# Kernel optimization log

Hardware: AMD Instinct MI355X
Metric: run time of the kernel (lower is better)

## Reference

```python
import jax, jax.numpy as jnp
import numpy as np

B, N, H, W = 8, 16384, 64, 64
CTX, OUT, ST = 32, 2, 1
HID = [516, 256, 128, 64, 32, 16]
IN_SIZE = CTX + 2 + ST + OUT  # 37


def _bilinear_sample(img, coord):
    """torch F.grid_sample, mode=bilinear, padding=zeros, align_corners=False.
    img: [B,C,H,W]; coord: [B,N,2] (x,y in [-1,1]). Returns [B,C,N]."""
    _, _, Hh, Ww = img.shape
    gx = (coord[..., 0] + 1.0) * (Ww * 0.5) - 0.5
    gy = (coord[..., 1] + 1.0) * (Hh * 0.5) - 0.5
    x0 = jnp.floor(gx)
    y0 = jnp.floor(gy)
    wx1 = gx - x0
    wy1 = gy - y0

    def tap(xi, yi, w):
        valid = (xi >= 0) & (xi < Ww) & (yi >= 0) & (yi < Hh)
        xc = jnp.clip(xi, 0, Ww - 1).astype(jnp.int32)
        yc = jnp.clip(yi, 0, Hh - 1).astype(jnp.int32)
        vals = jax.vmap(lambda im, y, x: im[:, y, x])(img, yc, xc)  # [B,C,N]
        return vals * (w * valid)[:, None, :]

    return (tap(x0, y0, (1 - wx1) * (1 - wy1))
            + tap(x0 + 1, y0, wx1 * (1 - wy1))
            + tap(x0, y0 + 1, (1 - wx1) * wy1)
            + tap(x0 + 1, y0 + 1, wx1 * wy1))


def _layer_shapes():
    shapes = [(IN_SIZE, HID[0])]
    for i in range(len(HID) - 1):
        shapes.append((HID[i] + IN_SIZE, HID[i + 1]))
    shapes.append((HID[-1], OUT))
    return shapes


def setup_inputs():
    key = jax.random.key(0)
    ks = jax.random.split(key, 4 + 7)
    inp = {
        "lr_fields": jax.random.normal(ks[0], (B, OUT, H, W), jnp.float32),
        "context_grid": jax.random.normal(ks[1], (B, CTX, H, W), jnp.float32),
        "hr_eps": jax.random.normal(ks[2], (B, H, W), jnp.float32),
        "coord": jax.random.uniform(ks[3], (B, N, 2), jnp.float32, -1.0, 1.0),
    }
    for j, (fi, fo) in enumerate(_layer_shapes()):
        inp[f"W{j}"] = jax.random.normal(ks[4 + j], (fi, fo), jnp.float32) / np.sqrt(fi)
        inp[f"b{j}"] = jnp.zeros((fo,), jnp.float32)
    return inp


def reference(lr_fields, context_grid, hr_eps, coord,
              W0, b0, W1, b1, W2, b2, W3, b3, W4, b4, W5, b5, W6, b6):
    # original permutes (0,1,3,2) before grid_sample -> swap spatial axes
    ctx_pts = _bilinear_sample(jnp.swapaxes(context_grid, 2, 3), coord)  # [B,CTX,N]
    lr_pts = _bilinear_sample(jnp.swapaxes(lr_fields, 2, 3), coord)      # [B,OUT,N]
    eps_pts = _bilinear_sample(jnp.swapaxes(hr_eps[:, None], 2, 3), coord)  # [B,1,N]
    x_in = jnp.concatenate([
        jnp.transpose(ctx_pts, (0, 2, 1)),
        coord,
        jnp.transpose(lr_pts, (0, 2, 1)),
        jnp.transpose(eps_pts, (0, 2, 1)),
    ], axis=2)  # [B,N,37]
    x = jax.nn.relu(x_in @ W0 + b0)
    for Wl, bl in ((W1, b1), (W2, b2), (W3, b3), (W4, b4), (W5, b5)):
        x = jax.nn.relu(jnp.concatenate([x, x_in], axis=2) @ Wl + bl)
    return x @ W6 + b6  # [B,N,2]
```

## Files before the change

### kernel.cpp

```cpp
#include <hip/hip_runtime.h>


#define NTH     1024
#define NWAVES  16
#define MPTS    64
#define MTILES  (MPTS / 16)
#define SROW    616
#define XIN_OFF 0
#define HSEG    64
#define NPOINTS (8 * 16384)
#define GRIDX   (NPOINTS / MPTS)
#define LDSBYTES (MPTS * SROW * 2)
#define CLSTRIDE 38
#define CLOFF   524288

typedef short          short8  __attribute__((ext_vector_type(8)));
typedef short          short4v __attribute__((ext_vector_type(4)));
typedef float          f32x4   __attribute__((ext_vector_type(4)));
typedef unsigned short u16;

__device__ __forceinline__ u16 f2bf(float f) {
    unsigned int u = __builtin_bit_cast(unsigned int, f);
    u += 0x7fffu + ((u >> 16) & 1u);
    return (u16)(u >> 16);
}

__constant__ int pk_base8[8] = {0, 4224, 23680, 28800, 30336, 30848, 31040, 31104};
__constant__ int pk_ks[7]    = {2, 19, 10, 6, 4, 3, 1};
__constant__ int pk_khp[7]   = {0, 544, 256, 128, 64, 32, 32};
__constant__ int pk_kact[7]  = {0, 516, 256, 128, 64, 32, 16};
__constant__ int pk_nact[7]  = {516, 256, 128, 64, 32, 16, 2};

struct WPtrs { const float* W[7]; };

__global__ void pack_weights(WPtrs wp, u16* __restrict__ out)
{
    const int f = blockIdx.x * blockDim.x + threadIdx.x;
    if (f >= 31104) return;
    int l = 0;
    while (l < 6 && f >= pk_base8[l + 1]) ++l;
    const int r    = f - pk_base8[l];
    const int lane = r & 63;
    const int t    = r >> 6;
    const int ks   = pk_ks[l];
    const int s    = t % ks;
    const int nt   = t / ks;
    const int n    = nt * 16 + (lane & 15);
    const int k0   = s * 32 + (lane >> 4) * 8;
    const int nact = pk_nact[l];
    const int khp  = pk_khp[l];
    const int kact = pk_kact[l];
    const float* W = wp.W[l];

    union { short8 v; u16 e[8]; } frag;
#pragma unroll
    for (int j = 0; j < 8; ++j) {
        const int k = k0 + j;
        float v = 0.0f;
        if (n < nact) {
            if (k < khp) {
                if (k < kact) v = W[k * nact + n];
            } else {
                const int xr = k - khp;
                if (xr < 37) v = W[(kact + xr) * nact + n];
            }
        }
        frag.e[j] = f2bf(v);
    }
    *(short8*)(out + (size_t)f * 8) = frag.v;
}

struct RPk { const float* ctx; const float* lr; const float* eps; float* cl; };

__global__ void repack_cl(RPk q)
{
    __shared__ float ls[64 * CLSTRIDE];
    const int b = blockIdx.x >> 6;
    const int x = blockIdx.x & 63;
    for (int i = threadIdx.x; i < 64 * CLSTRIDE; i += 256) ls[i] = 0.f;
    __syncthreads();
    for (int i = threadIdx.x; i < 35 * 64; i += 256) {
        const int c = i / 64, y = i % 64;
        float v; int slot;
        if (c < 32)      { v = q.ctx[(((size_t)b * 32 + c) * 64 + x) * 64 + y]; slot = c; }
        else if (c < 34) { v = q.lr [(((size_t)b * 2 + (c - 32)) * 64 + x) * 64 + y]; slot = 34 + (c - 32); }
        else             { v = q.eps[(((size_t)b) * 64 + x) * 64 + y];          slot = 36; }
        ls[y * CLSTRIDE + slot] = v;
    }
    __syncthreads();
    float* out = q.cl + ((size_t)b * 64 + x) * 64 * CLSTRIDE;
    for (int i = threadIdx.x; i < 64 * CLSTRIDE; i += 256) out[i] = ls[i];
}

struct MainParams {
    const float* lr;
    const float* ctx;
    const float* eps;
    const float* coord;
    const float* Bb[7];
    const u16*   wpack;
    const float* cl;
    int          clok;
    float*       out;
};

template<int NACT, bool RELU>
__device__ __forceinline__ void store_nt(const f32x4* accm,
                                         const float* __restrict__ bias,
                                         u16* __restrict__ s_act,
                                         int nt, int mbase, int lm, int lq)
{
    const int bn = nt * 16 + lq * 4;
    float bv[4];
    if (bn + 4 <= NACT) {
        const f32x4 b4 = *(const f32x4*)(bias + bn);
        bv[0] = b4[0]; bv[1] = b4[1]; bv[2] = b4[2]; bv[3] = b4[3];
    } else {
#pragma unroll
        for (int r = 0; r < 4; ++r)
            bv[r] = (bn + r < NACT) ? bias[bn + r] : 0.f;
    }
#pragma unroll
    for (int m = 0; m < 2; ++m) {
        short4v o;
#pragma unroll
        for (int r = 0; r < 4; ++r) {
            float v = accm[m][r] + bv[r];
            if (RELU) v = fmaxf(v, 0.f);
            o[r] = (short)f2bf(v);
        }
        *(short4v*)(s_act + (size_t)((mbase + m) * 16 + lm) * SROW + HSEG + bn) = o;
    }
}

template<int KHP, int NT, int NACT, int LBASE,
         bool XIN, bool RELU, bool GOUT, bool IPBAR>
__device__ __forceinline__ void mlayer(const u16* __restrict__ wpack,
                                       const float* __restrict__ bias,
                                       u16* __restrict__ s_act,
                                       float* __restrict__ gout, int p0,
                                       int wave, int lane)
{
    constexpr int KHS = KHP / 32;
    constexpr int KS  = KHS + (XIN ? 2 : 0);
    const int lm = lane & 15;
    const int lq = lane >> 4;
    const int mg = wave & 1;
    const int ng = wave >> 1;
    const int mbase = mg * 2;

    const u16* arow0 = s_act + (size_t)((mbase * 16) + lm) * SROW + lq * 8;
    const u16* arow1 = arow0 + (size_t)16 * SROW;
    const u16* wl = wpack + LBASE + lane * 8;

#define ABOFF(s_) (((s_) < KHS) ? (HSEG + (s_) * 32) : (XIN_OFF + ((s_) - KHS) * 32))

    if constexpr (IPBAR) {
        const int nt0 = ng, nt1 = ng + 8;
        const bool act0 = nt0 < NT;
        const bool act1 = nt1 < NT;
        f32x4 acc[2][2];
#pragma unroll
        for (int i = 0; i < 2; ++i)
#pragma unroll
            for (int m = 0; m < 2; ++m)
                acc[i][m] = (f32x4){0.f, 0.f, 0.f, 0.f};

        if (act0) {
            const u16* bp0 = wl + (size_t)nt0 * KS * 512;
            const u16* bp1 = wl + (size_t)nt1 * KS * 512;
#pragma unroll
            for (int s = 0; s < KS; ++s) {
                const int ab = ABOFF(s);
                const short8 a0 = *(const short8*)(arow0 + ab);
                const short8 a1 = *(const short8*)(arow1 + ab);
                const short8 w0 = *(const short8*)(bp0 + (size_t)s * 512);
                acc[0][0] = __builtin_amdgcn_mfma_f32_16x16x32_bf16(w0, a0, acc[0][0], 0, 0, 0);
                acc[0][1] = __builtin_amdgcn_mfma_f32_16x16x32_bf16(w0, a1, acc[0][1], 0, 0, 0);
                if (act1) {
                    const short8 w1 = *(const short8*)(bp1 + (size_t)s * 512);
                    acc[1][0] = __builtin_amdgcn_mfma_f32_16x16x32_bf16(w1, a0, acc[1][0], 0, 0, 0);
                    acc[1][1] = __builtin_amdgcn_mfma_f32_16x16x32_bf16(w1, a1, acc[1][1], 0, 0, 0);
                }
            }
        }
        __syncthreads();
        if (act0) store_nt<NACT, RELU>(acc[0], bias, s_act, nt0, mbase, lm, lq);
        if (act1) store_nt<NACT, RELU>(acc[1], bias, s_act, nt1, mbase, lm, lq);
    } else {
        for (int g = 0;; ++g) {
            const int nt0 = ng + 16 * g;
            if (nt0 >= NT) break;
            const int nt1 = nt0 + 8;
            const bool act1 = nt1 < NT;
            f32x4 acc[2][2];
#pragma unroll
            for (int i = 0; i < 2; ++i)
#pragma unroll
                for (int m = 0; m < 2; ++m)
                    acc[i][m] = (f32x4){0.f, 0.f, 0.f, 0.f};

            const u16* bp0 = wl + (size_t)nt0 * KS * 512;
            const u16* bp1 = wl + (size_t)nt1 * KS * 512;
#pragma unroll
            for (int s = 0; s < KS; ++s) {
                const int ab = ABOFF(s);
                const short8 a0 = *(const short8*)(arow0 + ab);
                const short8 a1 = *(const short8*)(arow1 + ab);
                const short8 w0 = *(const short8*)(bp0 + (size_t)s * 512);
                acc[0][0] = __builtin_amdgcn_mfma_f32_16x16x32_bf16(w0, a0, acc[0][0], 0, 0, 0);
                acc[0][1] = __builtin_amdgcn_mfma_f32_16x16x32_bf16(w0, a1, acc[0][1], 0, 0, 0);
                if (act1) {
                    const short8 w1 = *(const short8*)(bp1 + (size_t)s * 512);
                    acc[1][0] = __builtin_amdgcn_mfma_f32_16x16x32_bf16(w1, a0, acc[1][0], 0, 0, 0);
                    acc[1][1] = __builtin_amdgcn_mfma_f32_16x16x32_bf16(w1, a1, acc[1][1], 0, 0, 0);
                }
            }

            if (GOUT) {
                if (lq == 0) {
                    const float b0 = bias[0], b1 = bias[1];
#pragma unroll
                    for (int m = 0; m < 2; ++m) {
                        float2 o;
                        o.x = acc[0][m][0] + b0;
                        o.y = acc[0][m][1] + b1;
                        *(float2*)(gout + (size_t)(p0 + (mbase + m) * 16 + lm) * 2) = o;
                    }
                }
            } else {
                store_nt<NACT, RELU>(acc[0], bias, s_act, nt0, mbase, lm, lq);
                if (act1)
                    store_nt<NACT, RELU>(acc[1], bias, s_act, nt1, mbase, lm, lq);
            }
        }
    }
#undef ABOFF
}

__global__ __launch_bounds__(NTH, 8)
void cont_decoder_mfma(MainParams p)
{
    extern __shared__ u16 s_act[];
    __shared__ int   s_x0[MPTS], s_y0[MPTS];
    __shared__ float s_wx[MPTS], s_wy[MPTS];

    const int tid  = threadIdx.x;
    const int wave = tid >> 6;
    const int lane = tid & 63;
    const int p0   = blockIdx.x * MPTS;
    const int b    = p0 >> 14;

    for (int i = tid; i < MPTS * 43; i += NTH) {
        const int pt = i / 43, c = i % 43;
        const int col = (c < 27) ? (37 + c) : (592 + (c - 27));
        s_act[pt * SROW + col] = 0;
    }

    if (tid < MPTS) {
        const int pt = p0 + tid;
        const float cx = p.coord[2 * pt];
        const float cy = p.coord[2 * pt + 1];
        const float gx = (cx + 1.0f) * 32.0f - 0.5f;
        const float gy = (cy + 1.0f) * 32.0f - 0.5f;
        const float fx0 = floorf(gx), fy0 = floorf(gy);
        s_x0[tid] = (int)fx0;
        s_y0[tid] = (int)fy0;
        s_wx[tid] = gx - fx0;
        s_wy[tid] = gy - fy0;
        s_act[tid * SROW + 32] = f2bf(cx);
        s_act[tid * SROW + 33] = f2bf(cy);
    }
    __syncthreads();

    if (p.clok) {
        const float* cl = p.cl + (size_t)b * 64 * 64 * CLSTRIDE;
        for (int idx = tid; idx < MPTS * 35; idx += NTH) {
            const int t = idx / 35;
            const int c = idx % 35;
            const int col = (c < 32) ? c : 34 + (c - 32);

            const int   x0 = s_x0[t], y0 = s_y0[t];
            const float wx = s_wx[t], wy = s_wy[t];
            const int x1 = x0 + 1, y1 = y0 + 1;
            const bool xv0 = (x0 >= 0) & (x0 < 64);
            const bool xv1 = (x1 >= 0) & (x1 < 64);
            const bool yv0 = (y0 >= 0) & (y0 < 64);
            const bool yv1 = (y1 >= 0) & (y1 < 64);
            const int xc0 = min(max(x0, 0), 63), xc1 = min(max(x1, 0), 63);
            const int yc0 = min(max(y0, 0), 63), yc1 = min(max(y1, 0), 63);

            const float w00 = (1.0f - wx) * (1.0f - wy) * ((xv0 && yv0) ? 1.0f : 0.0f);
            const float w10 = wx * (1.0f - wy)          * ((xv1 && yv0) ? 1.0f : 0.0f);
            const float w01 = (1.0f - wx) * wy          * ((xv0 && yv1) ? 1.0f : 0.0f);
            const float w11 = wx * wy                   * ((xv1 && yv1) ? 1.0f : 0.0f);

            const float val = w00 * cl[(size_t)(xc0 * 64 + yc0) * CLSTRIDE + col]
                            + w10 * cl[(size_t)(xc1 * 64 + yc0) * CLSTRIDE + col]
                            + w01 * cl[(size_t)(xc0 * 64 + yc1) * CLSTRIDE + col]
                            + w11 * cl[(size_t)(xc1 * 64 + yc1) * CLSTRIDE + col];
            s_act[t * SROW + col] = f2bf(val);
        }
    } else {
        for (int idx = tid; idx < MPTS * 35; idx += NTH) {
            const int t = idx / 35;
            const int c = idx % 35;
            const float* base;
            int col;
            if (c < 32)      { base = p.ctx + (size_t)(b * 32 + c) * 4096;       col = c; }
            else if (c < 34) { base = p.lr  + (size_t)(b * 2 + (c - 32)) * 4096; col = 34 + (c - 32); }
            else             { base = p.eps + (size_t)b * 4096;                   col = 36; }

            const int   x0 = s_x0[t], y0 = s_y0[t];
            const float wx = s_wx[t], wy = s_wy[t];
            const int x1 = x0 + 1, y1 = y0 + 1;
            const bool xv0 = (x0 >= 0) & (x0 < 64);
            const bool xv1 = (x1 >= 0) & (x1 < 64);
            const bool yv0 = (y0 >= 0) & (y0 < 64);
            const bool yv1 = (y1 >= 0) & (y1 < 64);
            const int xc0 = min(max(x0, 0), 63), xc1 = min(max(x1, 0), 63);
            const int yc0 = min(max(y0, 0), 63), yc1 = min(max(y1, 0), 63);

            const float w00 = (1.0f - wx) * (1.0f - wy) * ((xv0 && yv0) ? 1.0f : 0.0f);
            const float w10 = wx * (1.0f - wy)          * ((xv1 && yv0) ? 1.0f : 0.0f);
            const float w01 = (1.0f - wx) * wy          * ((xv0 && yv1) ? 1.0f : 0.0f);
            const float w11 = wx * wy                   * ((xv1 && yv1) ? 1.0f : 0.0f);

            const float val = w00 * base[xc0 * 64 + yc0]
                            + w10 * base[xc1 * 64 + yc0]
                            + w01 * base[xc0 * 64 + yc1]
                            + w11 * base[xc1 * 64 + yc1];
            s_act[t * SROW + col] = f2bf(val);
        }
    }
    __syncthreads();

    mlayer<  0, 33, 516, 0,      true,  true,  false, false>(p.wpack, p.Bb[0], s_act, nullptr, p0, wave, lane);
    __syncthreads();
    mlayer<544, 16, 256, 33792,  true,  true,  false, true >(p.wpack, p.Bb[1], s_act, nullptr, p0, wave, lane);
    __syncthreads();
    mlayer<256,  8, 128, 189440, true,  true,  false, true >(p.wpack, p.Bb[2], s_act, nullptr, p0, wave, lane);
    __syncthreads();
    mlayer<128,  4,  64, 230400, true,  true,  false, true >(p.wpack, p.Bb[3], s_act, nullptr, p0, wave, lane);
    __syncthreads();
    mlayer< 64,  2,  32, 242688, true,  true,  false, true >(p.wpack, p.Bb[4], s_act, nullptr, p0, wave, lane);
    __syncthreads();
    mlayer< 32,  1,  16, 246784, true,  true,  false, true >(p.wpack, p.Bb[5], s_act, nullptr, p0, wave, lane);
    __syncthreads();
    mlayer< 32,  1,   2, 248320, false, false, true,  false>(p.wpack, p.Bb[6], s_act, p.out,   p0, wave, lane);
}

extern "C" void kernel_launch(void* const* d_in, const int* in_sizes, int n_in,
                              void* d_out, int out_size, void* d_ws, size_t ws_size,
                              hipStream_t stream)
{
    WPtrs wp;
    for (int l = 0; l < 7; ++l) wp.W[l] = (const float*)d_in[4 + 2 * l];

    const size_t cl_bytes = (size_t)8 * 64 * 64 * CLSTRIDE * 4;
    const bool clok = ws_size >= (size_t)CLOFF + cl_bytes;

    MainParams p;
    p.lr    = (const float*)d_in[0];
    p.ctx   = (const float*)d_in[1];
    p.eps   = (const float*)d_in[2];
    p.coord = (const float*)d_in[3];
    for (int l = 0; l < 7; ++l) p.Bb[l] = (const float*)d_in[5 + 2 * l];
    p.wpack = (const u16*)d_ws;
    p.cl    = (const float*)((const char*)d_ws + CLOFF);
    p.clok  = clok ? 1 : 0;
    p.out   = (float*)d_out;

    hipFuncSetAttribute((const void*)cont_decoder_mfma,
                        hipFuncAttributeMaxDynamicSharedMemorySize, LDSBYTES);

    hipLaunchKernelGGL(pack_weights, dim3(122), dim3(256), 0, stream, wp, (u16*)d_ws);
    if (clok) {
        RPk q;
        q.ctx = p.ctx; q.lr = p.lr; q.eps = p.eps;
        q.cl  = (float*)((char*)d_ws + CLOFF);
        hipLaunchKernelGGL(repack_cl, dim3(512), dim3(256), 0, stream, q);
    }
    hipLaunchKernelGGL(cont_decoder_mfma, dim3(GRIDX), dim3(NTH), LDSBYTES, stream, p);
}
```

Measured before the change: 187.0 us.

## Vectorize channels-last gather with float4 loads and use packed bf16 conversion

```diff
diff --git a/kernel.cpp b/kernel.cpp
--- a/kernel.cpp
+++ b/kernel.cpp
@@ -11,7 +11,7 @@
 #define NPOINTS (8 * 16384)
 #define GRIDX   (NPOINTS / MPTS)
 #define LDSBYTES (MPTS * SROW * 2)
-#define CLSTRIDE 38
+#define CLSTRIDE 40
 #define CLOFF   524288
 
 typedef short          short8  __attribute__((ext_vector_type(8)));
@@ -23,6 +23,12 @@
     unsigned int u = __builtin_bit_cast(unsigned int, f);
     u += 0x7fffu + ((u >> 16) & 1u);
     return (u16)(u >> 16);
+}
+
+__device__ __forceinline__ unsigned cvtpk(float a, float b) {
+    unsigned r;
+    asm("v_cvt_pk_bf16_f32 %0, %1, %2" : "=v"(r) : "v"(a), "v"(b));
+    return r;
 }
 
 __constant__ int pk_base8[8] = {0, 4224, 23680, 28800, 30336, 30848, 31040, 31104};
@@ -122,14 +128,16 @@
     }
 #pragma unroll
     for (int m = 0; m < 2; ++m) {
-        short4v o;
+        float v[4];
 #pragma unroll
         for (int r = 0; r < 4; ++r) {
-            float v = accm[m][r] + bv[r];
-            if (RELU) v = fmaxf(v, 0.f);
-            o[r] = (short)f2bf(v);
-        }
-        *(short4v*)(s_act + (size_t)((mbase + m) * 16 + lm) * SROW + HSEG + bn) = o;
+            v[r] = accm[m][r] + bv[r];
+            if (RELU) v[r] = fmaxf(v[r], 0.f);
+        }
+        uint2 o;
+        o.x = cvtpk(v[0], v[1]);
+        o.y = cvtpk(v[2], v[3]);
+        *(uint2*)(s_act + (size_t)((mbase + m) * 16 + lm) * SROW + HSEG + bn) = o;
     }
 }
 
@@ -275,10 +283,9 @@
 
     if (p.clok) {
         const float* cl = p.cl + (size_t)b * 64 * 64 * CLSTRIDE;
-        for (int idx = tid; idx < MPTS * 35; idx += NTH) {
-            const int t = idx / 35;
-            const int c = idx % 35;
-            const int col = (c < 32) ? c : 34 + (c - 32);
+        for (int idx = tid; idx < MPTS * 10; idx += NTH) {
+            const int t = idx / 10;
+            const int q = idx % 10;
 
             const int   x0 = s_x0[t], y0 = s_y0[t];
             const float wx = s_wx[t], wy = s_wy[t];
@@ -295,11 +302,22 @@
             const float w01 = (1.0f - wx) * wy          * ((xv0 && yv1) ? 1.0f : 0.0f);
             const float w11 = wx * wy                   * ((xv1 && yv1) ? 1.0f : 0.0f);
 
-            const float val = w00 * cl[(size_t)(xc0 * 64 + yc0) * CLSTRIDE + col]
-                            + w10 * cl[(size_t)(xc1 * 64 + yc0) * CLSTRIDE + col]
-                            + w01 * cl[(size_t)(xc0 * 64 + yc1) * CLSTRIDE + col]
-                            + w11 * cl[(size_t)(xc1 * 64 + yc1) * CLSTRIDE + col];
-            s_act[t * SROW + col] = f2bf(val);
+            const int qo = q * 4;
+            const f32x4 t00 = *(const f32x4*)(cl + (size_t)(xc0 * 64 + yc0) * CLSTRIDE + qo);
+            const f32x4 t10 = *(const f32x4*)(cl + (size_t)(xc1 * 64 + yc0) * CLSTRIDE + qo);
+            const f32x4 t01 = *(const f32x4*)(cl + (size_t)(xc0 * 64 + yc1) * CLSTRIDE + qo);
+            const f32x4 t11 = *(const f32x4*)(cl + (size_t)(xc1 * 64 + yc1) * CLSTRIDE + qo);
+
+            const f32x4 v = w00 * t00 + w10 * t10 + w01 * t01 + w11 * t11;
+            const unsigned lo = cvtpk(v[0], v[1]);
+            const unsigned hi = cvtpk(v[2], v[3]);
+
+            if (q == 8) {
+                *(unsigned*)(s_act + (size_t)t * SROW + 34) = hi;
+            } else {
+                uint2 o; o.x = lo; o.y = hi;
+                *(uint2*)(s_act + (size_t)t * SROW + qo) = o;
+            }
         }
     } else {
         for (int idx = tid; idx < MPTS * 35; idx += NTH) {
```

Result: no change. 184.4 us (-1.4%).
